# Kernel tuning notes

Hardware: AMD Instinct MI355X
Metric: run time of the kernel (lower is better)

Reference implementation:

```python
import jax, jax.numpy as jnp
import numpy as np

B, S, E, DK = 4, 4096, 512, 64

def setup_inputs() -> dict:
    key = jax.random.key(0)
    ks = jax.random.split(key, 5)
    x = jax.random.normal(ks[0], (B, S, E), dtype=jnp.float32)
    context = jax.random.normal(ks[1], (B, S, E), dtype=jnp.float32)
    Wq = jax.random.normal(ks[2], (E, DK), dtype=jnp.float32) * 0.02
    Wk = jax.random.normal(ks[3], (E, DK), dtype=jnp.float32) * 0.02
    Wv = jax.random.normal(ks[4], (E, DK), dtype=jnp.float32) * 0.02
    return {"x": x, "context": context, "Wq": Wq, "Wk": Wk, "Wv": Wv}

def reference(x, context, Wq, Wk, Wv):
    # pad mask: 1 where the token embedding in x is not all-zero  [B,S,1]
    mask = 1.0 - jnp.all(x == 0, axis=2, keepdims=True).astype(x.dtype)
    Q = (x @ Wq) * mask          # [B,S,dk]
    K = (context @ Wk) * mask    # [B,S,dk]
    V = (context @ Wv) * mask    # [B,S,dk]
    energy = jnp.einsum('bqd,bkd->bqk', Q, K)  # [B,S,S]
    # original per-batch loop: length = #nonzero entries in first query row,
    # then columns >= length set to -inf (assumes trailing padding)
    lengths = jnp.sum(energy[:, 0, :] != 0, axis=-1)            # [B]
    col_valid = jnp.arange(S)[None, :] < lengths[:, None]       # [B,S]
    energy = jnp.where(col_valid[:, None, :], energy, -jnp.inf)
    score = jax.nn.softmax(energy / jnp.sqrt(jnp.asarray(DK, x.dtype)), axis=-1)
    return jnp.einsum('bqk,bkd->bqd', score, V) * mask
```

## Files before the change

### kernel.cpp

```cpp
#include <hip/hip_runtime.h>

constexpr int BB = 4;
constexpr int SS = 4096;
constexpr int EE = 512;
constexpr int BS = BB * SS;

typedef __attribute__((ext_vector_type(8))) short bf16x8;
typedef __attribute__((ext_vector_type(4))) float f32x4;
typedef unsigned long long ull;

union Frag {
  uint4 u4;
  unsigned int u[4];
  bf16x8 v;
};

__device__ __forceinline__ unsigned short f2bf(float f) {
  union { float f; unsigned int u; } v; v.f = f;
  unsigned int r = v.u + 0x7FFFu + ((v.u >> 16) & 1u);
  return (unsigned short)(r >> 16);
}
__device__ __forceinline__ float bf2f(unsigned short h) {
  union { unsigned int u; float f; } v; v.u = ((unsigned int)h) << 16;
  return v.f;
}
__device__ __forceinline__ unsigned int packbf(float a, float b) {
  return (unsigned int)f2bf(a) | ((unsigned int)f2bf(b) << 16);
}

__global__ __launch_bounds__(256) void mask_kernel(const float* __restrict__ x,
                                                   float* __restrict__ maskp) {
  const int row = blockIdx.x * 4 + (threadIdx.x >> 6);
  const int l = threadIdx.x & 63;
  const uint4* xr = (const uint4*)(x + (size_t)row * EE) + l;
  uint4 a = xr[0], b = xr[64];
  unsigned int o = (a.x | a.y | a.z | a.w | b.x | b.y | b.z | b.w) << 1;
  bool nz = __any(o != 0u);
  if (l == 0) maskp[row] = nz ? 1.0f : 0.0f;
}

__global__ __launch_bounds__(256) void proj_kernel(
    const float* __restrict__ x, const float* __restrict__ ctx,
    const float* __restrict__ Wq, const float* __restrict__ Wk,
    const float* __restrict__ Wv, const float* __restrict__ maskp,
    unsigned short* __restrict__ Qb, unsigned short* __restrict__ Kb,
    unsigned short* __restrict__ Vt)
{
  __shared__ __align__(16) float At[2][32][68];
  __shared__ __align__(16) float Wl[2][32][64];

  const int t = threadIdx.x;
  const int z = blockIdx.y;
  const int r0g = blockIdx.x * 64;

  const float* A = (z == 0) ? x : ctx;
  const float* W = (z == 0) ? Wq : (z == 1) ? Wk : Wv;

  const int arow = t >> 3;
  const int ak   = (t & 7) << 2;
  const int wk   = t >> 4;
  const int wc   = (t & 15) << 2;

  float4 ar0, ar1, wv0, wv1;
  auto stage_load = [&](int kc) {
    ar0 = *(const float4*)(A + (size_t)(r0g + arow) * EE + kc + ak);
    ar1 = *(const float4*)(A + (size_t)(r0g + arow + 32) * EE + kc + ak);
    wv0 = *(const float4*)(W + (size_t)(kc + wk) * 64 + wc);
    wv1 = *(const float4*)(W + (size_t)(kc + wk + 16) * 64 + wc);
  };
  auto stage_write = [&](int buf) {
    At[buf][ak + 0][arow] = ar0.x; At[buf][ak + 1][arow] = ar0.y;
    At[buf][ak + 2][arow] = ar0.z; At[buf][ak + 3][arow] = ar0.w;
    At[buf][ak + 0][arow + 32] = ar1.x; At[buf][ak + 1][arow + 32] = ar1.y;
    At[buf][ak + 2][arow + 32] = ar1.z; At[buf][ak + 3][arow + 32] = ar1.w;
    *(float4*)&Wl[buf][wk][wc] = wv0;
    *(float4*)&Wl[buf][wk + 16][wc] = wv1;
  };

  const int r0 = (t & 15) << 2;
  const int c0 = (t >> 4) << 2;
  float acc[4][4] = {};

  stage_load(0);
  stage_write(0);
  int cur = 0;
  for (int c = 0; c < 16; ++c) {
    if (c < 15) stage_load((c + 1) * 32);
    __syncthreads();
#pragma unroll 8
    for (int kk = 0; kk < 32; ++kk) {
      float4 av = *(const float4*)&At[cur][kk][r0];
      float4 wv = *(const float4*)&Wl[cur][kk][c0];
      acc[0][0] = fmaf(av.x, wv.x, acc[0][0]); acc[0][1] = fmaf(av.x, wv.y, acc[0][1]);
      acc[0][2] = fmaf(av.x, wv.z, acc[0][2]); acc[0][3] = fmaf(av.x, wv.w, acc[0][3]);
      acc[1][0] = fmaf(av.y, wv.x, acc[1][0]); acc[1][1] = fmaf(av.y, wv.y, acc[1][1]);
      acc[1][2] = fmaf(av.y, wv.z, acc[1][2]); acc[1][3] = fmaf(av.y, wv.w, acc[1][3]);
      acc[2][0] = fmaf(av.z, wv.x, acc[2][0]); acc[2][1] = fmaf(av.z, wv.y, acc[2][1]);
      acc[2][2] = fmaf(av.z, wv.z, acc[2][2]); acc[2][3] = fmaf(av.z, wv.w, acc[2][3]);
      acc[3][0] = fmaf(av.w, wv.x, acc[3][0]); acc[3][1] = fmaf(av.w, wv.y, acc[3][1]);
      acc[3][2] = fmaf(av.w, wv.z, acc[3][2]); acc[3][3] = fmaf(av.w, wv.w, acc[3][3]);
    }
    __syncthreads();
    if (c < 15) stage_write(cur ^ 1);
    cur ^= 1;
  }

  float mk[4];
#pragma unroll
  for (int i = 0; i < 4; ++i) mk[i] = maskp[r0g + r0 + i];
  if (z == 2) {
    const int b = r0g >> 12;
    const int sl = (r0g & 4095) + r0;
#pragma unroll
    for (int j = 0; j < 4; ++j) {
      ull v = (ull)f2bf(acc[0][j] * mk[0])
            | ((ull)f2bf(acc[1][j] * mk[1]) << 16)
            | ((ull)f2bf(acc[2][j] * mk[2]) << 32)
            | ((ull)f2bf(acc[3][j] * mk[3]) << 48);
      *(ull*)(Vt + ((size_t)(b * 64 + c0 + j)) * SS + sl) = v;
    }
  } else {
    unsigned short* O = (z == 0) ? Qb : Kb;
#pragma unroll
    for (int i = 0; i < 4; ++i) {
      ull v = (ull)f2bf(acc[i][0] * mk[i])
            | ((ull)f2bf(acc[i][1] * mk[i]) << 16)
            | ((ull)f2bf(acc[i][2] * mk[i]) << 32)
            | ((ull)f2bf(acc[i][3] * mk[i]) << 48);
      *(ull*)(O + (size_t)(r0g + r0 + i) * 64 + c0) = v;
    }
  }
}

__global__ __launch_bounds__(256) void len_kernel(
    const unsigned short* __restrict__ Qb,
    const unsigned short* __restrict__ Kb,
    unsigned int* __restrict__ lenp)
{
  __shared__ float q0row[64];
  const int t = threadIdx.x;
  const int b = blockIdx.y;
  if (t < 64) q0row[t] = bf2f(Qb[(size_t)b * SS * 64 + t]);
  __syncthreads();
  const int k = blockIdx.x * 256 + t;
  const unsigned short* kr = Kb + ((size_t)(b * SS + k)) * 64;
  float acc = 0.f;
#pragma unroll
  for (int d = 0; d < 64; ++d) acc = fmaf(q0row[d], bf2f(kr[d]), acc);
  unsigned long long bal = __ballot(acc != 0.0f);
  if ((t & 63) == 0) atomicAdd(&lenp[b], (unsigned int)__popcll(bal));
}

__global__ __launch_bounds__(256) void attn_kernel(
    const unsigned short* __restrict__ Qb,
    const unsigned short* __restrict__ Kb,
    const unsigned short* __restrict__ Vt,
    const unsigned int* __restrict__ lenp,
    float* __restrict__ Op, float* __restrict__ mlp, int nsplit)
{
  __shared__ __align__(16) unsigned int ks[2][2048];
  __shared__ __align__(16) unsigned int vs[2][2048];
  __shared__ __align__(16) unsigned int ps[4 * 16 * 36];

  const int t  = threadIdx.x;
  const int l  = t & 63;
  const int wi = t >> 6;
  const int g  = l >> 4;
  const int li = l & 15;
  const int b  = blockIdx.z;
  const int sp = blockIdx.y;
  const int q0 = blockIdx.x * 64;

  const unsigned int len = lenp[b];
  const int kvChunk = SS / nsplit;
  const int kvS = sp * kvChunk;
  const int kvE = min((int)len, kvS + kvChunk);
  const int NT  = max(0, (kvE - kvS + 63) >> 6);

  Frag qf0, qf1;
  {
    const uint4* qg = (const uint4*)(Qb + ((size_t)(b * SS + q0 + wi * 16 + li)) * 64);
    qf0.u4 = qg[g]; qf1.u4 = qg[4 + g];
  }

  f32x4 O[4] = {};
  float m_r = -1e30f, l_r = 0.f;

  const int srow = t >> 3;
  const int sch  = t & 7;
  uint4 kr0, kr1, vr0, vr1;
  auto stage_load = [&](int key0) {
    const unsigned short* Kbase = Kb + ((size_t)(b * SS + key0)) * 64;
    kr0 = *(const uint4*)(Kbase + (size_t)srow * 64 + sch * 8);
    kr1 = *(const uint4*)(Kbase + (size_t)(srow + 32) * 64 + sch * 8);
    const unsigned short* Vbase = Vt + (size_t)b * 64 * SS + key0;
    vr0 = *(const uint4*)(Vbase + (size_t)srow * SS + sch * 8);
    vr1 = *(const uint4*)(Vbase + (size_t)(srow + 32) * SS + sch * 8);
  };
  auto stage_write = [&](int buf) {
    *(uint4*)&ks[buf][srow * 32 + ((sch ^ (srow & 7)) << 2)] = kr0;
    *(uint4*)&ks[buf][(srow + 32) * 32 + ((sch ^ (srow & 7)) << 2)] = kr1;
    *(uint4*)&vs[buf][srow * 32 + ((sch ^ (srow & 7)) << 2)] = vr0;
    *(uint4*)&vs[buf][(srow + 32) * 32 + ((sch ^ (srow & 7)) << 2)] = vr1;
  };

  int cur = 0;
  if (NT > 0) { stage_load(kvS); stage_write(0); }
  for (int tix = 0; tix < NT; ++tix) {
    const int key0 = kvS + tix * 64;
    if (tix + 1 < NT) stage_load(key0 + 64);
    __syncthreads();

    f32x4 acc[4] = {};
#pragma unroll
    for (int f = 0; f < 2; ++f) {
      const bf16x8 qv = f ? qf1.v : qf0.v;
      const int oc = f * 4 + g;
#pragma unroll
      for (int a = 0; a < 4; ++a) {
        const int krow = a * 16 + li;
        Frag kf; kf.u4 = *(const uint4*)&ks[cur][krow * 32 + ((oc ^ (krow & 7)) << 2)];
        acc[a] = __builtin_amdgcn_mfma_f32_16x16x32_bf16(kf.v, qv, acc[a], 0, 0, 0);
      }
    }

    const float SC = 0.18033688011112042f;
    const int lim = kvE - key0;
    float pv[4][4];
    float tm = -1e30f;
#pragma unroll
    for (int a = 0; a < 4; ++a)
#pragma unroll
      for (int r = 0; r < 4; ++r) {
        const int kk = a * 16 + (g << 2) + r;
        const float v = (kk < lim) ? acc[a][r] * SC : -1e30f;
        pv[a][r] = v; tm = fmaxf(tm, v);
      }
    tm = fmaxf(tm, __shfl_xor(tm, 16));
    tm = fmaxf(tm, __shfl_xor(tm, 32));
    if (__any(tm > m_r + 8.f)) {
      const float nm = fmaxf(m_r, tm);
      const float al = exp2f(m_r - nm);
      m_r = nm; l_r *= al;
      float alq[4];
#pragma unroll
      for (int r = 0; r < 4; ++r) alq[r] = __shfl(al, (l & 48) | (g << 2) | r);
#pragma unroll
      for (int o4 = 0; o4 < 4; ++o4)
#pragma unroll
        for (int r = 0; r < 4; ++r) O[o4][r] *= alq[r];
    }
    float rs = 0.f;
#pragma unroll
    for (int a = 0; a < 4; ++a)
#pragma unroll
      for (int r = 0; r < 4; ++r) { const float e = exp2f(pv[a][r] - m_r); pv[a][r] = e; rs += e; }
    rs += __shfl_xor(rs, 16);
    rs += __shfl_xor(rs, 32);
    l_r += rs;

    unsigned int* prow = &ps[(wi * 16 + li) * 36];
#pragma unroll
    for (int a = 0; a < 4; ++a) {
      prow[a * 8 + g * 2 + 0] = packbf(pv[a][0], pv[a][1]);
      prow[a * 8 + g * 2 + 1] = packbf(pv[a][2], pv[a][3]);
    }
#pragma unroll
    for (int f = 0; f < 2; ++f) {
      Frag pf; pf.u4 = *(const uint4*)&prow[f * 16 + g * 4];
      const int oc = f * 4 + g;
#pragma unroll
      for (int o4 = 0; o4 < 4; ++o4) {
        const int vrow = o4 * 16 + li;
        Frag vf; vf.u4 = *(const uint4*)&vs[cur][vrow * 32 + ((oc ^ (vrow & 7)) << 2)];
        O[o4] = __builtin_amdgcn_mfma_f32_16x16x32_bf16(pf.v, vf.v, O[o4], 0, 0, 0);
      }
    }
    __syncthreads();
    if (tix + 1 < NT) stage_write(cur ^ 1);
    cur ^= 1;
  }

  const int qrow = q0 + wi * 16;
  if (g == 0) {
    mlp[(size_t)sp * 2 * BS + b * SS + qrow + li] = m_r;
    mlp[(size_t)sp * 2 * BS + BS + b * SS + qrow + li] = l_r;
  }
  const size_t obase = (size_t)sp * BS * 64;
#pragma unroll
  for (int o4 = 0; o4 < 4; ++o4)
#pragma unroll
    for (int r = 0; r < 4; ++r)
      Op[obase + ((size_t)(b * SS + qrow + (g << 2) + r)) * 64 + o4 * 16 + li] = O[o4][r];
}

__global__ __launch_bounds__(256) void combine_kernel(
    const float* __restrict__ Op, const float* __restrict__ mlp,
    const float* __restrict__ maskp, float* __restrict__ out, int nsplit)
{
  const int e = blockIdx.x * 256 + threadIdx.x;
  const int row = e >> 6;
  const float m0 = mlp[row], l0 = mlp[BS + row];
  const float o0 = Op[e];
  float res;
  if (nsplit == 2) {
    const float m1 = mlp[2 * BS + row], l1 = mlp[3 * BS + row];
    const float o1 = Op[(size_t)BS * 64 + e];
    const float M = fmaxf(m0, m1);
    const float w0 = (l0 > 0.f) ? exp2f(m0 - M) : 0.f;
    const float w1 = (l1 > 0.f) ? exp2f(m1 - M) : 0.f;
    const float lt = w0 * l0 + w1 * l1;
    const float sc = (lt > 0.f) ? maskp[row] / lt : 0.f;
    res = (w0 * o0 + w1 * o1) * sc;
  } else {
    res = (l0 > 0.f) ? o0 * (maskp[row] / l0) : 0.f;
  }
  out[e] = res;
}

extern "C" void kernel_launch(void* const* d_in, const int* in_sizes, int n_in,
                              void* d_out, int out_size, void* d_ws, size_t ws_size,
                              hipStream_t stream) {
  const float* x   = (const float*)d_in[0];
  const float* ctx = (const float*)d_in[1];
  const float* Wq  = (const float*)d_in[2];
  const float* Wk  = (const float*)d_in[3];
  const float* Wv  = (const float*)d_in[4];
  float* out = (float*)d_out;

  char* ws = (char*)d_ws;
  unsigned short* Qb = (unsigned short*)(ws);
  unsigned short* Kb = (unsigned short*)(ws + 2097152);
  unsigned short* Vt = (unsigned short*)(ws + 4194304);
  float* maskp       = (float*)(ws + 6291456);
  unsigned int* lenp = (unsigned int*)(ws + 6356992);
  float* Op          = (float*)(ws + 6357248);

  const size_t need2 = 6357248ull + 8388608ull + 262144ull;
  const int nsplit = (ws_size >= need2) ? 2 : 1;
  float* mlp = (float*)(ws + 6357248 + (size_t)nsplit * 4194304);

  hipMemsetAsync(lenp, 0, 16, stream);
  mask_kernel<<<dim3(BS / 4), 256, 0, stream>>>(x, maskp);
  proj_kernel<<<dim3(BS / 64, 3), 256, 0, stream>>>(x, ctx, Wq, Wk, Wv, maskp, Qb, Kb, Vt);
  len_kernel<<<dim3(16, 4), 256, 0, stream>>>(Qb, Kb, lenp);
  attn_kernel<<<dim3(SS / 64, nsplit, BB), 256, 0, stream>>>(Qb, Kb, Vt, lenp, Op, mlp, nsplit);
  combine_kernel<<<dim3(BS * 64 / 256), 256, 0, stream>>>(Op, mlp, maskp, out, nsplit);
}
```

Measured before the change: 211.8 us.

## Use split-bf16 MFMA projection, async LDS loads and 4-way KV split attention

The projection kernel moves from scalar fp32 FMA to MFMA, using a hi/lo bf16 split (three products) to keep near-fp32 accuracy. K and V are now projected in one pass that reads ctx once, and the softmax scale is folded into Wq. The attention kernel loads K/V tiles straight into LDS with global_load_lds, splits the KV range 4 ways with 8 waves per block, and uses a mask-free path for full tiles. It also adds the cvt_pk_bf16 packing instruction, vectorises the length and combine kernels, and needs more workspace for the extra partial outputs.

```diff
diff --git a/kernel.cpp b/kernel.cpp
--- a/kernel.cpp
+++ b/kernel.cpp
@@ -16,16 +16,40 @@
 };
 
 __device__ __forceinline__ unsigned short f2bf(float f) {
-  union { float f; unsigned int u; } v; v.f = f;
-  unsigned int r = v.u + 0x7FFFu + ((v.u >> 16) & 1u);
+  unsigned int u = __float_as_uint(f);
+  unsigned int r = u + 0x7FFFu + ((u >> 16) & 1u);
   return (unsigned short)(r >> 16);
 }
 __device__ __forceinline__ float bf2f(unsigned short h) {
-  union { unsigned int u; float f; } v; v.u = ((unsigned int)h) << 16;
-  return v.f;
-}
-__device__ __forceinline__ unsigned int packbf(float a, float b) {
-  return (unsigned int)f2bf(a) | ((unsigned int)f2bf(b) << 16);
+  return __uint_as_float(((unsigned int)h) << 16);
+}
+__device__ __forceinline__ unsigned int cvtpk(float a, float b) {
+  unsigned int r;
+  asm("v_cvt_pk_bf16_f32 %0, %1, %2" : "=v"(r) : "v"(a), "v"(b));
+  return r;
+}
+__device__ __forceinline__ void gl16(const unsigned short* g, unsigned int* l) {
+  __builtin_amdgcn_global_load_lds(
+      (const __attribute__((address_space(1))) unsigned int*)(size_t)g,
+      (__attribute__((address_space(3))) unsigned int*)(unsigned int)(size_t)l,
+      16, 0, 0);
+}
+#define WAITVM(n) asm volatile("s_waitcnt vmcnt(" #n ")" ::: "memory")
+
+__device__ __forceinline__ void split8(const float* v, uint4& H, uint4& L) {
+  unsigned int hu[4], lu[4];
+#pragma unroll
+  for (int i = 0; i < 4; ++i) {
+    unsigned int u0 = __float_as_uint(v[2 * i]);
+    unsigned int u1 = __float_as_uint(v[2 * i + 1]);
+    unsigned int h0 = u0 & 0xFFFF0000u, h1 = u1 & 0xFFFF0000u;
+    hu[i] = (u0 >> 16) | h1;
+    unsigned int r0 = __float_as_uint(v[2 * i] - __uint_as_float(h0));
+    unsigned int r1 = __float_as_uint(v[2 * i + 1] - __uint_as_float(h1));
+    lu[i] = (r0 >> 16) | (r1 & 0xFFFF0000u);
+  }
+  H = make_uint4(hu[0], hu[1], hu[2], hu[3]);
+  L = make_uint4(lu[0], lu[1], lu[2], lu[3]);
 }
 
 __global__ __launch_bounds__(256) void mask_kernel(const float* __restrict__ x,
@@ -39,96 +63,108 @@
   if (l == 0) maskp[row] = nz ? 1.0f : 0.0f;
 }
 
-__global__ __launch_bounds__(256) void proj_kernel(
+__global__ __launch_bounds__(256, 2) void proj_kernel(
     const float* __restrict__ x, const float* __restrict__ ctx,
     const float* __restrict__ Wq, const float* __restrict__ Wk,
     const float* __restrict__ Wv, const float* __restrict__ maskp,
     unsigned short* __restrict__ Qb, unsigned short* __restrict__ Kb,
     unsigned short* __restrict__ Vt)
 {
-  __shared__ __align__(16) float At[2][32][68];
-  __shared__ __align__(16) float Wl[2][32][64];
+  __shared__ __align__(16) unsigned short Ah[2][64][40], Al[2][64][40];
+  __shared__ __align__(16) unsigned short Wh[2][128][40], Wl[2][128][40];
 
   const int t = threadIdx.x;
-  const int z = blockIdx.y;
+  const int kvmode = blockIdx.y;
   const int r0g = blockIdx.x * 64;
-
-  const float* A = (z == 0) ? x : ctx;
-  const float* W = (z == 0) ? Wq : (z == 1) ? Wk : Wv;
-
-  const int arow = t >> 3;
-  const int ak   = (t & 7) << 2;
-  const int wk   = t >> 4;
-  const int wc   = (t & 15) << 2;
-
-  float4 ar0, ar1, wv0, wv1;
-  auto stage_load = [&](int kc) {
-    ar0 = *(const float4*)(A + (size_t)(r0g + arow) * EE + kc + ak);
-    ar1 = *(const float4*)(A + (size_t)(r0g + arow + 32) * EE + kc + ak);
-    wv0 = *(const float4*)(W + (size_t)(kc + wk) * 64 + wc);
-    wv1 = *(const float4*)(W + (size_t)(kc + wk + 16) * 64 + wc);
+  const int nlim = kvmode ? 8 : 4;
+
+  const float* A = kvmode ? ctx : x;
+
+  const int arow = t >> 2, akq = t & 3;
+  const int wn = t & 127, wkq = t >> 7;
+  const int wn6 = wn & 63;
+  const float* Wg = kvmode ? ((wn < 64) ? Wk : Wv) : Wq;
+  const float wscale = kvmode ? 1.0f : 0.18033688011112042f;
+  const bool wact = kvmode || (wn < 64);
+
+  float a8[8], w16[16];
+  auto sload = [&](int kc) {
+    const float* ap = A + (size_t)(r0g + arow) * EE + kc + akq * 8;
+    *(float4*)&a8[0] = *(const float4*)ap;
+    *(float4*)&a8[4] = *(const float4*)(ap + 4);
+    if (wact) {
+#pragma unroll
+      for (int j = 0; j < 16; ++j)
+        w16[j] = Wg[(size_t)(kc + wkq * 16 + j) * 64 + wn6] * wscale;
+    }
   };
-  auto stage_write = [&](int buf) {
-    At[buf][ak + 0][arow] = ar0.x; At[buf][ak + 1][arow] = ar0.y;
-    At[buf][ak + 2][arow] = ar0.z; At[buf][ak + 3][arow] = ar0.w;
-    At[buf][ak + 0][arow + 32] = ar1.x; At[buf][ak + 1][arow + 32] = ar1.y;
-    At[buf][ak + 2][arow + 32] = ar1.z; At[buf][ak + 3][arow + 32] = ar1.w;
-    *(float4*)&Wl[buf][wk][wc] = wv0;
-    *(float4*)&Wl[buf][wk + 16][wc] = wv1;
+  auto swrite = [&](int buf) {
+    uint4 H, L;
+    split8(a8, H, L);
+    *(uint4*)&Ah[buf][arow][akq * 8] = H;
+    *(uint4*)&Al[buf][arow][akq * 8] = L;
+    if (wact) {
+      split8(w16, H, L);
+      *(uint4*)&Wh[buf][wn][wkq * 16] = H;
+      *(uint4*)&Wl[buf][wn][wkq * 16] = L;
+      split8(w16 + 8, H, L);
+      *(uint4*)&Wh[buf][wn][wkq * 16 + 8] = H;
+      *(uint4*)&Wl[buf][wn][wkq * 16 + 8] = L;
+    }
   };
 
-  const int r0 = (t & 15) << 2;
-  const int c0 = (t >> 4) << 2;
-  float acc[4][4] = {};
-
-  stage_load(0);
-  stage_write(0);
+  const int l = t & 63, wi = t >> 6, g = l >> 4, li = l & 15;
+  f32x4 acc[8] = {};
+
+  sload(0);
+  swrite(0);
   int cur = 0;
   for (int c = 0; c < 16; ++c) {
-    if (c < 15) stage_load((c + 1) * 32);
+    if (c < 15) sload((c + 1) * 32);
     __syncthreads();
-#pragma unroll 8
-    for (int kk = 0; kk < 32; ++kk) {
-      float4 av = *(const float4*)&At[cur][kk][r0];
-      float4 wv = *(const float4*)&Wl[cur][kk][c0];
-      acc[0][0] = fmaf(av.x, wv.x, acc[0][0]); acc[0][1] = fmaf(av.x, wv.y, acc[0][1]);
-      acc[0][2] = fmaf(av.x, wv.z, acc[0][2]); acc[0][3] = fmaf(av.x, wv.w, acc[0][3]);
-      acc[1][0] = fmaf(av.y, wv.x, acc[1][0]); acc[1][1] = fmaf(av.y, wv.y, acc[1][1]);
-      acc[1][2] = fmaf(av.y, wv.z, acc[1][2]); acc[1][3] = fmaf(av.y, wv.w, acc[1][3]);
-      acc[2][0] = fmaf(av.z, wv.x, acc[2][0]); acc[2][1] = fmaf(av.z, wv.y, acc[2][1]);
-      acc[2][2] = fmaf(av.z, wv.z, acc[2][2]); acc[2][3] = fmaf(av.z, wv.w, acc[2][3]);
-      acc[3][0] = fmaf(av.w, wv.x, acc[3][0]); acc[3][1] = fmaf(av.w, wv.y, acc[3][1]);
-      acc[3][2] = fmaf(av.w, wv.z, acc[3][2]); acc[3][3] = fmaf(av.w, wv.w, acc[3][3]);
-    }
-    __syncthreads();
-    if (c < 15) stage_write(cur ^ 1);
+    Frag ah, alo;
+    ah.u4  = *(const uint4*)&Ah[cur][wi * 16 + li][g * 8];
+    alo.u4 = *(const uint4*)&Al[cur][wi * 16 + li][g * 8];
+#pragma unroll
+    for (int nf = 0; nf < 8; ++nf) {
+      if (nf < nlim) {
+        Frag bh, bl;
+        bh.u4 = *(const uint4*)&Wh[cur][nf * 16 + li][g * 8];
+        bl.u4 = *(const uint4*)&Wl[cur][nf * 16 + li][g * 8];
+        acc[nf] = __builtin_amdgcn_mfma_f32_16x16x32_bf16(ah.v, bh.v, acc[nf], 0, 0, 0);
+        acc[nf] = __builtin_amdgcn_mfma_f32_16x16x32_bf16(alo.v, bh.v, acc[nf], 0, 0, 0);
+        acc[nf] = __builtin_amdgcn_mfma_f32_16x16x32_bf16(ah.v, bl.v, acc[nf], 0, 0, 0);
+      }
+    }
+    if (c < 15) swrite(cur ^ 1);
     cur ^= 1;
   }
 
   float mk[4];
-#pragma unroll
-  for (int i = 0; i < 4; ++i) mk[i] = maskp[r0g + r0 + i];
-  if (z == 2) {
-    const int b = r0g >> 12;
-    const int sl = (r0g & 4095) + r0;
-#pragma unroll
-    for (int j = 0; j < 4; ++j) {
-      ull v = (ull)f2bf(acc[0][j] * mk[0])
-            | ((ull)f2bf(acc[1][j] * mk[1]) << 16)
-            | ((ull)f2bf(acc[2][j] * mk[2]) << 32)
-            | ((ull)f2bf(acc[3][j] * mk[3]) << 48);
-      *(ull*)(Vt + ((size_t)(b * 64 + c0 + j)) * SS + sl) = v;
+  const int browbase = r0g + wi * 16 + g * 4;
+#pragma unroll
+  for (int r = 0; r < 4; ++r) mk[r] = maskp[browbase + r];
+  if (kvmode) {
+#pragma unroll
+    for (int nf = 0; nf < 4; ++nf)
+#pragma unroll
+      for (int r = 0; r < 4; ++r)
+        Kb[(size_t)(browbase + r) * 64 + nf * 16 + li] = f2bf(acc[nf][r] * mk[r]);
+    const int bidx = r0g >> 12;
+    const int sbase = (r0g & 4095) + wi * 16 + g * 4;
+#pragma unroll
+    for (int nf = 4; nf < 8; ++nf) {
+      unsigned int u0 = cvtpk(acc[nf][0] * mk[0], acc[nf][1] * mk[1]);
+      unsigned int u1 = cvtpk(acc[nf][2] * mk[2], acc[nf][3] * mk[3]);
+      ull v = (ull)u0 | ((ull)u1 << 32);
+      *(ull*)(Vt + ((size_t)(bidx * 64 + (nf - 4) * 16 + li)) * SS + sbase) = v;
     }
   } else {
-    unsigned short* O = (z == 0) ? Qb : Kb;
-#pragma unroll
-    for (int i = 0; i < 4; ++i) {
-      ull v = (ull)f2bf(acc[i][0] * mk[i])
-            | ((ull)f2bf(acc[i][1] * mk[i]) << 16)
-            | ((ull)f2bf(acc[i][2] * mk[i]) << 32)
-            | ((ull)f2bf(acc[i][3] * mk[i]) << 48);
-      *(ull*)(O + (size_t)(r0g + r0 + i) * 64 + c0) = v;
-    }
+#pragma unroll
+    for (int nf = 0; nf < 4; ++nf)
+#pragma unroll
+      for (int r = 0; r < 4; ++r)
+        Qb[(size_t)(browbase + r) * 64 + nf * 16 + li] = f2bf(acc[nf][r] * mk[r]);
   }
 }
 
@@ -143,24 +179,114 @@
   if (t < 64) q0row[t] = bf2f(Qb[(size_t)b * SS * 64 + t]);
   __syncthreads();
   const int k = blockIdx.x * 256 + t;
-  const unsigned short* kr = Kb + ((size_t)(b * SS + k)) * 64;
+  const uint4* kr = (const uint4*)(Kb + ((size_t)(b * SS + k)) * 64);
   float acc = 0.f;
 #pragma unroll
-  for (int d = 0; d < 64; ++d) acc = fmaf(q0row[d], bf2f(kr[d]), acc);
+  for (int j = 0; j < 8; ++j) {
+    uint4 u = kr[j];
+    unsigned int w[4] = {u.x, u.y, u.z, u.w};
+#pragma unroll
+    for (int q = 0; q < 4; ++q) {
+      acc = fmaf(q0row[j * 8 + q * 2],     __uint_as_float(w[q] << 16), acc);
+      acc = fmaf(q0row[j * 8 + q * 2 + 1], __uint_as_float(w[q] & 0xFFFF0000u), acc);
+    }
+  }
   unsigned long long bal = __ballot(acc != 0.0f);
   if ((t & 63) == 0) atomicAdd(&lenp[b], (unsigned int)__popcll(bal));
 }
 
-__global__ __launch_bounds__(256) void attn_kernel(
+template <bool MASKED>
+__device__ __forceinline__ void tile_body(
+    const unsigned int* ksb, const unsigned int* vsb, unsigned int* prow,
+    const Frag& qf0, const Frag& qf1, f32x4* O, float& m_r, float& l_r,
+    int l, int g, int li, int lim)
+{
+  f32x4 acc[4] = {};
+#pragma unroll
+  for (int f = 0; f < 2; ++f) {
+    const bf16x8 qv = f ? qf1.v : qf0.v;
+    const int oc = f * 4 + g;
+#pragma unroll
+    for (int a = 0; a < 4; ++a) {
+      const int krow = a * 16 + li;
+      Frag kf;
+      kf.u4 = *(const uint4*)&ksb[krow * 32 + ((oc ^ (krow & 7)) << 2)];
+      acc[a] = __builtin_amdgcn_mfma_f32_16x16x32_bf16(kf.v, qv, acc[a], 0, 0, 0);
+    }
+  }
+
+  float pvv[4][4];
+  float tm = -1e30f;
+#pragma unroll
+  for (int a = 0; a < 4; ++a)
+#pragma unroll
+    for (int r = 0; r < 4; ++r) {
+      float v = acc[a][r];
+      if (MASKED) v = (a * 16 + (g << 2) + r < lim) ? v : -1e30f;
+      pvv[a][r] = v;
+      tm = fmaxf(tm, v);
+    }
+  if (__any(tm > m_r + 8.f)) {
+    float tq = fmaxf(tm, __shfl_xor(tm, 16));
+    tq = fmaxf(tq, __shfl_xor(tq, 32));
+    const float nm = fmaxf(m_r, tq);
+    const float al = exp2f(m_r - nm);
+    m_r = nm;
+    l_r *= al;
+    float alq[4];
+#pragma unroll
+    for (int r = 0; r < 4; ++r) alq[r] = __shfl(al, (l & 48) | (g << 2) | r);
+#pragma unroll
+    for (int o4 = 0; o4 < 4; ++o4)
+#pragma unroll
+      for (int r = 0; r < 4; ++r) O[o4][r] *= alq[r];
+  }
+  float rs = 0.f;
+#pragma unroll
+  for (int a = 0; a < 4; ++a)
+#pragma unroll
+    for (int r = 0; r < 4; ++r) {
+      float e = exp2f(pvv[a][r] - m_r);
+      pvv[a][r] = e;
+      rs += e;
+    }
+  rs += __shfl_xor(rs, 16);
+  rs += __shfl_xor(rs, 32);
+  l_r += rs;
+
+#pragma unroll
+  for (int a = 0; a < 4; ++a) {
+    prow[a * 8 + g * 2]     = cvtpk(pvv[a][0], pvv[a][1]);
+    prow[a * 8 + g * 2 + 1] = cvtpk(pvv[a][2], pvv[a][3]);
+  }
+#pragma unroll
+  for (int f = 0; f < 2; ++f) {
+    Frag pf;
+    pf.u4 = *(const uint4*)&prow[f * 16 + g * 4];
+    const int oc = f * 4 + g;
+#pragma unroll
+    for (int o4 = 0; o4 < 4; ++o4) {
+      const int vrow = o4 * 16 + li;
+      Frag vf;
+      vf.u4 = *(const uint4*)&vsb[vrow * 32 + ((oc ^ (vrow & 7)) << 2)];
+      O[o4] = __builtin_amdgcn_mfma_f32_16x16x32_bf16(pf.v, vf.v, O[o4], 0, 0, 0);
+    }
+  }
+}
+
+template <int NW>
+__global__ __launch_bounds__(NW * 64, (NW == 8) ? 4 : 3) void attn_kernel(
     const unsigned short* __restrict__ Qb,
     const unsigned short* __restrict__ Kb,
     const unsigned short* __restrict__ Vt,
     const unsigned int* __restrict__ lenp,
-    float* __restrict__ Op, float* __restrict__ mlp, int nsplit)
+    float* __restrict__ Op, float* __restrict__ mlp, int kvChunk)
 {
   __shared__ __align__(16) unsigned int ks[2][2048];
   __shared__ __align__(16) unsigned int vs[2][2048];
-  __shared__ __align__(16) unsigned int ps[4 * 16 * 36];
+  __shared__ __align__(16) unsigned int ps[NW * 16 * 36];
+
+  constexpr int SPW = 16 / NW;
 
   const int t  = threadIdx.x;
   const int l  = t & 63;
@@ -169,115 +295,63 @@
   const int li = l & 15;
   const int b  = blockIdx.z;
   const int sp = blockIdx.y;
-  const int q0 = blockIdx.x * 64;
+  const int q0 = blockIdx.x * (NW * 16);
 
   const unsigned int len = lenp[b];
-  const int kvChunk = SS / nsplit;
   const int kvS = sp * kvChunk;
   const int kvE = min((int)len, kvS + kvChunk);
-  const int NT  = max(0, (kvE - kvS + 63) >> 6);
+  int rem = kvE - kvS; if (rem < 0) rem = 0;
+  const int NF = rem >> 6;
+  const int NT = NF + ((rem & 63) ? 1 : 0);
 
   Frag qf0, qf1;
   {
     const uint4* qg = (const uint4*)(Qb + ((size_t)(b * SS + q0 + wi * 16 + li)) * 64);
-    qf0.u4 = qg[g]; qf1.u4 = qg[4 + g];
+    qf0.u4 = qg[g];
+    qf1.u4 = qg[4 + g];
   }
 
   f32x4 O[4] = {};
-  float m_r = -1e30f, l_r = 0.f;
-
-  const int srow = t >> 3;
-  const int sch  = t & 7;
-  uint4 kr0, kr1, vr0, vr1;
-  auto stage_load = [&](int key0) {
-    const unsigned short* Kbase = Kb + ((size_t)(b * SS + key0)) * 64;
-    kr0 = *(const uint4*)(Kbase + (size_t)srow * 64 + sch * 8);
-    kr1 = *(const uint4*)(Kbase + (size_t)(srow + 32) * 64 + sch * 8);
-    const unsigned short* Vbase = Vt + (size_t)b * 64 * SS + key0;
-    vr0 = *(const uint4*)(Vbase + (size_t)srow * SS + sch * 8);
-    vr1 = *(const uint4*)(Vbase + (size_t)(srow + 32) * SS + sch * 8);
+  float m_r = 0.f, l_r = 0.f;
+
+  const int srow8 = l >> 3;
+  const int sch = l & 7;
+  auto issue = [&](int key0, int bufsel) {
+#pragma unroll
+    for (int s2 = 0; s2 < SPW; ++s2) {
+      const int seg = wi * SPW + s2;
+      const int s8 = seg & 7;
+      const int row = s8 * 8 + srow8;
+      if (seg < 8) {
+        gl16(Kb + ((size_t)(b * SS + key0 + row)) * 64 + ((sch ^ (row & 7)) << 3),
+             &ks[bufsel][s8 * 256]);
+      } else {
+        gl16(Vt + ((size_t)(b * 64 + row)) * SS + key0 + ((sch ^ (row & 7)) << 3),
+             &vs[bufsel][s8 * 256]);
+      }
+    }
   };
-  auto stage_write = [&](int buf) {
-    *(uint4*)&ks[buf][srow * 32 + ((sch ^ (srow & 7)) << 2)] = kr0;
-    *(uint4*)&ks[buf][(srow + 32) * 32 + ((sch ^ (srow & 7)) << 2)] = kr1;
-    *(uint4*)&vs[buf][srow * 32 + ((sch ^ (srow & 7)) << 2)] = vr0;
-    *(uint4*)&vs[buf][(srow + 32) * 32 + ((sch ^ (srow & 7)) << 2)] = vr1;
-  };
-
+
+  unsigned int* prow = &ps[(wi * 16 + li) * 36];
   int cur = 0;
-  if (NT > 0) { stage_load(kvS); stage_write(0); }
+  if (NT > 0) issue(kvS, 0);
   for (int tix = 0; tix < NT; ++tix) {
-    const int key0 = kvS + tix * 64;
-    if (tix + 1 < NT) stage_load(key0 + 64);
-    __syncthreads();
-
-    f32x4 acc[4] = {};
-#pragma unroll
-    for (int f = 0; f < 2; ++f) {
-      const bf16x8 qv = f ? qf1.v : qf0.v;
-      const int oc = f * 4 + g;
-#pragma unroll
-      for (int a = 0; a < 4; ++a) {
-        const int krow = a * 16 + li;
-        Frag kf; kf.u4 = *(const uint4*)&ks[cur][krow * 32 + ((oc ^ (krow & 7)) << 2)];
-        acc[a] = __builtin_amdgcn_mfma_f32_16x16x32_bf16(kf.v, qv, acc[a], 0, 0, 0);
-      }
-    }
-
-    const float SC = 0.18033688011112042f;
+    const int key0 = kvS + (tix << 6);
+    const bool last = (tix + 1 == NT);
+    if (!last) {
+      issue(key0 + 64, cur ^ 1);
+      if constexpr (NW == 8) { WAITVM(2); } else { WAITVM(4); }
+    } else {
+      WAITVM(0);
+    }
+    __builtin_amdgcn_s_barrier();
+    __builtin_amdgcn_sched_barrier(0);
     const int lim = kvE - key0;
-    float pv[4][4];
-    float tm = -1e30f;
-#pragma unroll
-    for (int a = 0; a < 4; ++a)
-#pragma unroll
-      for (int r = 0; r < 4; ++r) {
-        const int kk = a * 16 + (g << 2) + r;
-        const float v = (kk < lim) ? acc[a][r] * SC : -1e30f;
-        pv[a][r] = v; tm = fmaxf(tm, v);
-      }
-    tm = fmaxf(tm, __shfl_xor(tm, 16));
-    tm = fmaxf(tm, __shfl_xor(tm, 32));
-    if (__any(tm > m_r + 8.f)) {
-      const float nm = fmaxf(m_r, tm);
-      const float al = exp2f(m_r - nm);
-      m_r = nm; l_r *= al;
-      float alq[4];
-#pragma unroll
-      for (int r = 0; r < 4; ++r) alq[r] = __shfl(al, (l & 48) | (g << 2) | r);
-#pragma unroll
-      for (int o4 = 0; o4 < 4; ++o4)
-#pragma unroll
-        for (int r = 0; r < 4; ++r) O[o4][r] *= alq[r];
-    }
-    float rs = 0.f;
-#pragma unroll
-    for (int a = 0; a < 4; ++a)
-#pragma unroll
-      for (int r = 0; r < 4; ++r) { const float e = exp2f(pv[a][r] - m_r); pv[a][r] = e; rs += e; }
-    rs += __shfl_xor(rs, 16);
-    rs += __shfl_xor(rs, 32);
-    l_r += rs;
-
-    unsigned int* prow = &ps[(wi * 16 + li) * 36];
-#pragma unroll
-    for (int a = 0; a < 4; ++a) {
-      prow[a * 8 + g * 2 + 0] = packbf(pv[a][0], pv[a][1]);
-      prow[a * 8 + g * 2 + 1] = packbf(pv[a][2], pv[a][3]);
-    }
-#pragma unroll
-    for (int f = 0; f < 2; ++f) {
-      Frag pf; pf.u4 = *(const uint4*)&prow[f * 16 + g * 4];
-      const int oc = f * 4 + g;
-#pragma unroll
-      for (int o4 = 0; o4 < 4; ++o4) {
-        const int vrow = o4 * 16 + li;
-        Frag vf; vf.u4 = *(const uint4*)&vs[cur][vrow * 32 + ((oc ^ (vrow & 7)) << 2)];
-        O[o4] = __builtin_amdgcn_mfma_f32_16x16x32_bf16(pf.v, vf.v, O[o4], 0, 0, 0);
-      }
-    }
-    __syncthreads();
-    if (tix + 1 < NT) stage_write(cur ^ 1);
+    if (tix < NF)
+      tile_body<false>(&ks[cur][0], &vs[cur][0], prow, qf0, qf1, O, m_r, l_r, l, g, li, lim);
+    else
+      tile_body<true>(&ks[cur][0], &vs[cur][0], prow, qf0, qf1, O, m_r, l_r, l, g, li, lim);
+    __builtin_amdgcn_s_barrier();
     cur ^= 1;
   }
 
@@ -294,28 +368,38 @@
       Op[obase + ((size_t)(b * SS + qrow + (g << 2) + r)) * 64 + o4 * 16 + li] = O[o4][r];
 }
 
+template <int NS>
 __global__ __launch_bounds__(256) void combine_kernel(
     const float* __restrict__ Op, const float* __restrict__ mlp,
-    const float* __restrict__ maskp, float* __restrict__ out, int nsplit)
+    const float* __restrict__ maskp, float* __restrict__ out)
 {
-  const int e = blockIdx.x * 256 + threadIdx.x;
-  const int row = e >> 6;
-  const float m0 = mlp[row], l0 = mlp[BS + row];
-  const float o0 = Op[e];
-  float res;
-  if (nsplit == 2) {
-    const float m1 = mlp[2 * BS + row], l1 = mlp[3 * BS + row];
-    const float o1 = Op[(size_t)BS * 64 + e];
-    const float M = fmaxf(m0, m1);
-    const float w0 = (l0 > 0.f) ? exp2f(m0 - M) : 0.f;
-    const float w1 = (l1 > 0.f) ? exp2f(m1 - M) : 0.f;
-    const float lt = w0 * l0 + w1 * l1;
-    const float sc = (lt > 0.f) ? maskp[row] / lt : 0.f;
-    res = (w0 * o0 + w1 * o1) * sc;
-  } else {
-    res = (l0 > 0.f) ? o0 * (maskp[row] / l0) : 0.f;
-  }
-  out[e] = res;
+  const int i4 = blockIdx.x * 256 + threadIdx.x;
+  const int e0 = i4 * 4;
+  const int row = e0 >> 6;
+  float ms[NS], lsv[NS];
+#pragma unroll
+  for (int s = 0; s < NS; ++s) {
+    ms[s] = mlp[(size_t)s * 2 * BS + row];
+    lsv[s] = mlp[(size_t)s * 2 * BS + BS + row];
+  }
+  float M = -1e30f;
+#pragma unroll
+  for (int s = 0; s < NS; ++s)
+    if (lsv[s] > 0.f) M = fmaxf(M, ms[s]);
+  float4 num = {0.f, 0.f, 0.f, 0.f};
+  float den = 0.f;
+#pragma unroll
+  for (int s = 0; s < NS; ++s) {
+    if (lsv[s] > 0.f) {
+      const float w = exp2f(ms[s] - M);
+      const float4 o = *(const float4*)(Op + (size_t)s * BS * 64 + e0);
+      num.x += w * o.x; num.y += w * o.y; num.z += w * o.z; num.w += w * o.w;
+      den += w * lsv[s];
+    }
+  }
+  const float sc = (den > 0.f) ? maskp[row] / den : 0.f;
+  float4 r = {num.x * sc, num.y * sc, num.z * sc, num.w * sc};
+  *(float4*)(out + e0) = r;
 }
 
 extern "C" void kernel_launch(void* const* d_in, const int* in_sizes, int n_in,
@@ -334,16 +418,27 @@
   unsigned short* Vt = (unsigned short*)(ws + 4194304);
   float* maskp       = (float*)(ws + 6291456);
   unsigned int* lenp = (unsigned int*)(ws + 6356992);
-  float* Op          = (float*)(ws + 6357248);
-
-  const size_t need2 = 6357248ull + 8388608ull + 262144ull;
-  const int nsplit = (ws_size >= need2) ? 2 : 1;
-  float* mlp = (float*)(ws + 6357248 + (size_t)nsplit * 4194304);
+  const size_t base = 6357248ull;
+
+  const size_t need4 = base + 4ull * 4194304 + 4ull * 131072;
+  const size_t need2 = base + 2ull * 4194304 + 2ull * 131072;
+  int nsplit = (ws_size >= need4) ? 4 : (ws_size >= need2) ? 2 : 1;
+
+  float* Op  = (float*)(ws + base);
+  float* mlp = (float*)(ws + base + (size_t)nsplit * 4194304);
 
   hipMemsetAsync(lenp, 0, 16, stream);
   mask_kernel<<<dim3(BS / 4), 256, 0, stream>>>(x, maskp);
-  proj_kernel<<<dim3(BS / 64, 3), 256, 0, stream>>>(x, ctx, Wq, Wk, Wv, maskp, Qb, Kb, Vt);
+  proj_kernel<<<dim3(BS / 64, 2), 256, 0, stream>>>(x, ctx, Wq, Wk, Wv, maskp, Qb, Kb, Vt);
   len_kernel<<<dim3(16, 4), 256, 0, stream>>>(Qb, Kb, lenp);
-  attn_kernel<<<dim3(SS / 64, nsplit, BB), 256, 0, stream>>>(Qb, Kb, Vt, lenp, Op, mlp, nsplit);
-  combine_kernel<<<dim3(BS * 64 / 256), 256, 0, stream>>>(Op, mlp, maskp, out, nsplit);
-}
+  if (nsplit == 4) {
+    attn_kernel<8><<<dim3(SS / 128, 4, BB), 512, 0, stream>>>(Qb, Kb, Vt, lenp, Op, mlp, 1024);
+    combine_kernel<4><<<dim3(BS * 64 / 1024), 256, 0, stream>>>(Op, mlp, maskp, out);
+  } else if (nsplit == 2) {
+    attn_kernel<4><<<dim3(SS / 64, 2, BB), 256, 0, stream>>>(Qb, Kb, Vt, lenp, Op, mlp, 2048);
+    combine_kernel<2><<<dim3(BS * 64 / 1024), 256, 0, stream>>>(Op, mlp, maskp, out);
+  } else {
+    attn_kernel<4><<<dim3(SS / 64, 1, BB), 256, 0, stream>>>(Qb, Kb, Vt, lenp, Op, mlp, 4096);
+    combine_kernel<1><<<dim3(BS * 64 / 1024), 256, 0, stream>>>(Op, mlp, maskp, out);
+  }
+}
```

Measured after the change: 170.0 us. -19.7%, faster.
